# Kernel optimization log

Hardware: AMD Instinct MI355X
Metric: run time of the kernel (lower is better)

## Reference

```python
import jax, jax.numpy as jnp
import numpy as np

B, N, D = 1, 768, 768
H, HD = 16, 48
ZD = 128
EPS = 1e-5


def layer_norm(x, w, b):
    mu = jnp.mean(x, axis=-1, keepdims=True)
    var = jnp.mean(jnp.square(x - mu), axis=-1, keepdims=True)
    return (x - mu) * jax.lax.rsqrt(var + EPS) * w + b


def setup_inputs() -> dict:
    key = jax.random.key(0)
    ks = jax.random.split(key, 16)
    sc = 0.02
    return {
        "s": jax.random.normal(ks[0], (B, N, D), jnp.float32),
        "z": jax.random.normal(ks[1], (B, N, N, ZD), jnp.float32),
        "norm_s_w": jnp.ones((D,), jnp.float32),
        "norm_s_b": jnp.zeros((D,), jnp.float32),
        "q_w": jax.random.normal(ks[2], (D, D), jnp.float32) * sc,
        "q_b": jax.random.normal(ks[3], (D,), jnp.float32) * sc,
        "k_w": jax.random.normal(ks[4], (D, D), jnp.float32) * sc,
        "v_w": jax.random.normal(ks[5], (D, D), jnp.float32) * sc,
        "g_w": jax.random.normal(ks[6], (D, D), jnp.float32) * sc,
        "z_norm_w": jnp.ones((ZD,), jnp.float32),
        "z_norm_b": jnp.zeros((ZD,), jnp.float32),
        "z_w": jax.random.normal(ks[7], (ZD, H), jnp.float32) * sc,
        "o_w": jax.random.normal(ks[8], (D, D), jnp.float32) * sc,
    }


def reference(s, z, norm_s_w, norm_s_b, q_w, q_b, k_w, v_w, g_w,
              z_norm_w, z_norm_b, z_w, o_w):
    # diffusion=False: pre layer-norm on s
    sn = layer_norm(s, norm_s_w, norm_s_b)                 # [B,N,D]
    q = (sn @ q_w + q_b).reshape(B, N, H, HD)              # split D -> (H, HD)
    k = (sn @ k_w).reshape(B, N, H, HD)
    v = (sn @ v_w).reshape(B, N, H, HD)
    scale = HD ** -0.5
    # scores: [H,B,Q,K]
    a = jnp.einsum('bqhd,bkhd->hbqk', q, k) * scale
    # pair bias from z: LayerNorm + Linear(ZD->H), permute to [H,B,N,N]
    zb = layer_norm(z, z_norm_w, z_norm_b) @ z_w           # [B,N,N,H]
    a = a + jnp.transpose(zb, (3, 0, 1, 2))
    a = jax.nn.softmax(a, axis=-1)
    o = jnp.einsum('hbqk,bkhd->bqhd', a, v).reshape(B, N, D)
    g = jax.nn.sigmoid(sn @ g_w)                           # gate
    return (o * g) @ o_w
```

## Files before the change

### kernel.cpp

```cpp
#include <hip/hip_runtime.h>
#include <math.h>

constexpr int NT = 768;
constexpr int DT = 768;
constexpr int HT = 16;
constexpr int HDT = 48;
constexpr int ZDT = 128;
constexpr int NN = NT * NT;
constexpr float LN_EPS = 1e-5f;
constexpr float SCALE = 0.14433756729740643f;
constexpr int KP = 72;

typedef __attribute__((ext_vector_type(8))) short bfrag;
typedef __attribute__((ext_vector_type(4))) float ffrag;

#define MFMA16(a, b, c) __builtin_amdgcn_mfma_f32_16x16x32_bf16(a, b, c, 0, 0, 0)

__device__ __forceinline__ short f2b(float f) {
  unsigned u = __builtin_bit_cast(unsigned, f);
  u += 0x7fffu + ((u >> 16) & 1u);
  return (short)(u >> 16);
}
__device__ __forceinline__ float b2f(short s) {
  return __builtin_bit_cast(float, (unsigned)(unsigned short)s << 16);
}

__global__ __launch_bounds__(256) void ln_s_kernel(
    const float* __restrict__ s, const float* __restrict__ w,
    const float* __restrict__ b, short* __restrict__ snb) {
  const int row = blockIdx.x;
  const int t = threadIdx.x;
  const float* x = s + row * DT;
  float v0 = x[t], v1 = x[t + 256], v2 = x[t + 512];
  float sum = v0 + v1 + v2;
  float sq = v0 * v0 + v1 * v1 + v2 * v2;
#pragma unroll
  for (int off = 32; off; off >>= 1) {
    sum += __shfl_xor(sum, off);
    sq += __shfl_xor(sq, off);
  }
  __shared__ float ls[4], lq[4], stats[2];
  const int wid = t >> 6;
  if ((t & 63) == 0) { ls[wid] = sum; lq[wid] = sq; }
  __syncthreads();
  if (t == 0) {
    float S = ls[0] + ls[1] + ls[2] + ls[3];
    float Q = lq[0] + lq[1] + lq[2] + lq[3];
    float mu = S * (1.f / DT);
    float var = Q * (1.f / DT) - mu * mu;
    stats[0] = mu;
    stats[1] = rsqrtf(var + LN_EPS);
  }
  __syncthreads();
  const float mu = stats[0], rs = stats[1];
  short* y = snb + row * DT;
  y[t] = f2b((v0 - mu) * rs * w[t] + b[t]);
  y[t + 256] = f2b((v1 - mu) * rs * w[t + 256] + b[t + 256]);
  y[t + 512] = f2b((v2 - mu) * rs * w[t + 512] + b[t + 512]);
}

__global__ __launch_bounds__(256) void prep_kernel(
    const float* __restrict__ qw, const float* __restrict__ kw,
    const float* __restrict__ vw, const float* __restrict__ gw,
    const float* __restrict__ ow, short* __restrict__ wt) {
  __shared__ float Ts[64][65];
  const int t = threadIdx.x;
  const int which = blockIdx.z;
  const float* src = which == 0 ? qw : which == 1 ? kw : which == 2 ? vw
                     : which == 3 ? gw : ow;
  short* dst = wt + (size_t)which * NN;
  const int k0 = blockIdx.y * 64;
  const int n0 = blockIdx.x * 64;
  const int r = t >> 4, c = (t & 15) * 4;
#pragma unroll
  for (int i = 0; i < 4; i++) {
    int rr = r + i * 16;
    float4 v = *(const float4*)&src[(size_t)(k0 + rr) * DT + n0 + c];
    Ts[rr][c + 0] = v.x; Ts[rr][c + 1] = v.y;
    Ts[rr][c + 2] = v.z; Ts[rr][c + 3] = v.w;
  }
  __syncthreads();
#pragma unroll
  for (int i = 0; i < 2; i++) {
    int cid = t + i * 256;
    int nr = cid >> 3, kc = cid & 7;
    union { uint4 u; short s2[8]; } pk;
#pragma unroll
    for (int j = 0; j < 8; j++) pk.s2[j] = f2b(Ts[kc * 8 + j][nr]);
    *(uint4*)&dst[(size_t)(n0 + nr) * DT + k0 + kc * 8] = pk.u;
  }
}

__global__ __launch_bounds__(256) void zsetup_kernel(
    const float* __restrict__ znw, const float* __restrict__ znb,
    const float* __restrict__ zw, float* __restrict__ w1,
    float* __restrict__ bh) {
  const int t = threadIdx.x;
#pragma unroll
  for (int i = 0; i < 8; i++) {
    int idx = t * 8 + i;
    int c = idx >> 4;
    w1[idx] = znw[c] * zw[idx];
  }
  if (t < HT) {
    float s = 0.f;
    for (int c = 0; c < ZDT; c++) s += znb[c] * zw[c * HT + t];
    bh[t] = s;
  }
}

__global__ __launch_bounds__(256) void zbias_kernel(
    const float* __restrict__ z, const float* __restrict__ w1,
    const float* __restrict__ bh, short* __restrict__ biasb) {
  const int t = threadIdx.x;
  const int slot = t >> 5;
  const int hq = (t >> 3) & 3;
  const int cg = t & 7;
  const int c0 = cg * 16;
  const int h0 = hq * 4;
  float4 Wr[16];
#pragma unroll
  for (int j = 0; j < 16; j++)
    Wr[j] = *(const float4*)&w1[(c0 + j) * HT + h0];
  const float4 B4 = *(const float4*)&bh[h0];
  const int row0 = blockIdx.x * 256;
  for (int it = 0; it < 32; it++) {
    const int rid = row0 + it * 8 + slot;
    const float* zp = &z[(size_t)rid * ZDT + c0];
    float x[16];
    *(float4*)&x[0] = *(const float4*)&zp[0];
    *(float4*)&x[4] = *(const float4*)&zp[4];
    *(float4*)&x[8] = *(const float4*)&zp[8];
    *(float4*)&x[12] = *(const float4*)&zp[12];
    float sum = 0.f, sq = 0.f;
#pragma unroll
    for (int j = 0; j < 16; j++) { sum += x[j]; sq += x[j] * x[j]; }
#pragma unroll
    for (int m = 1; m <= 4; m <<= 1) {
      sum += __shfl_xor(sum, m);
      sq += __shfl_xor(sq, m);
    }
    const float mu = sum * (1.f / 128.f);
    const float rs = rsqrtf(sq * (1.f / 128.f) - mu * mu + LN_EPS);
    float ax = 0.f, ay = 0.f, az = 0.f, aw = 0.f;
#pragma unroll
    for (int j = 0; j < 16; j++) {
      float xc = x[j] - mu;
      ax += xc * Wr[j].x; ay += xc * Wr[j].y;
      az += xc * Wr[j].z; aw += xc * Wr[j].w;
    }
#pragma unroll
    for (int m = 1; m <= 4; m <<= 1) {
      ax += __shfl_xor(ax, m); ay += __shfl_xor(ay, m);
      az += __shfl_xor(az, m); aw += __shfl_xor(aw, m);
    }
    if (cg == 0) {
      biasb[(size_t)(h0 + 0) * NN + rid] = f2b(ax * rs + B4.x);
      biasb[(size_t)(h0 + 1) * NN + rid] = f2b(ay * rs + B4.y);
      biasb[(size_t)(h0 + 2) * NN + rid] = f2b(az * rs + B4.z);
      biasb[(size_t)(h0 + 3) * NN + rid] = f2b(aw * rs + B4.w);
    }
  }
}

__global__ __launch_bounds__(256) void proj_kernel(
    const short* __restrict__ snb, const short* __restrict__ wt,
    const float* __restrict__ qbias, short* __restrict__ qb,
    short* __restrict__ kb, short* __restrict__ vT, short* __restrict__ gb) {
  __shared__ short As[128 * KP];
  __shared__ short Bs[128 * KP];
  const int t = threadIdx.x;
  const int which = blockIdx.z;
  const short* W = wt + (size_t)which * NN;
  const int N0 = blockIdx.x * 128;
  const int M0 = blockIdx.y * 128;
  const int w = t >> 6, l = t & 63;
  const int wm = (w >> 1) * 64, wn = (w & 1) * 64;
  const int lane16 = l & 15, quad = l >> 4;
  ffrag acc[4][4] = {};
  const int srow = t >> 3, skc = t & 7;
  for (int k0 = 0; k0 < DT; k0 += 64) {
    uint4 av[4], bv[4];
#pragma unroll
    for (int i = 0; i < 4; i++) {
      int row = srow + i * 32;
      av[i] = *(const uint4*)&snb[(size_t)(M0 + row) * DT + k0 + skc * 8];
      bv[i] = *(const uint4*)&W[(size_t)(N0 + row) * DT + k0 + skc * 8];
    }
    __syncthreads();
#pragma unroll
    for (int i = 0; i < 4; i++) {
      int row = srow + i * 32;
      *(uint4*)&As[row * KP + skc * 8] = av[i];
      *(uint4*)&Bs[row * KP + skc * 8] = bv[i];
    }
    __syncthreads();
#pragma unroll
    for (int ks = 0; ks < 2; ks++) {
      bfrag a[4], b[4];
#pragma unroll
      for (int i = 0; i < 4; i++)
        a[i] = *(const bfrag*)&As[(wm + i * 16 + lane16) * KP + ks * 32 + quad * 8];
#pragma unroll
      for (int j = 0; j < 4; j++)
        b[j] = *(const bfrag*)&Bs[(wn + j * 16 + lane16) * KP + ks * 32 + quad * 8];
#pragma unroll
      for (int i = 0; i < 4; i++)
#pragma unroll
        for (int j = 0; j < 4; j++) acc[i][j] = MFMA16(a[i], b[j], acc[i][j]);
    }
    __syncthreads();
  }
#pragma unroll
  for (int i = 0; i < 4; i++) {
#pragma unroll
    for (int j = 0; j < 4; j++) {
      int n = N0 + wn + j * 16 + lane16;
#pragma unroll
      for (int r = 0; r < 4; r++) {
        int m = M0 + wm + i * 16 + quad * 4 + r;
        float v = acc[i][j][r];
        if (which == 0) {
          qb[(size_t)m * DT + n] = f2b(v + qbias[n]);
        } else if (which == 1) {
          kb[(size_t)m * DT + n] = f2b(v);
        } else if (which == 2) {
          vT[(size_t)n * NT + m] = f2b(v);
        } else {
          gb[(size_t)m * DT + n] = f2b(1.f / (1.f + __expf(-v)));
        }
      }
    }
  }
}

__global__ __launch_bounds__(256) void attn_kernel(
    const short* __restrict__ qb, const short* __restrict__ kb,
    const short* __restrict__ vT, const short* __restrict__ biasb,
    float* __restrict__ oX) {
  __shared__ short Ks[128 * 48];
  __shared__ short Vs[48 * 136];
  __shared__ short Ps[4][16 * 136];
  const int t = threadIdx.x;
  const int h = blockIdx.y;
  const int q0 = blockIdx.x * 64;
  const int w = t >> 6, l = t & 63;
  const int lane16 = l & 15, quad = l >> 4;
  const int qrow = q0 + w * 16 + lane16;
  bfrag a_q0 = *(const bfrag*)&qb[(size_t)qrow * DT + h * HDT + quad * 8];
  bfrag a_q1 = {0, 0, 0, 0, 0, 0, 0, 0};
  if (quad < 2)
    a_q1 = *(const bfrag*)&qb[(size_t)qrow * DT + h * HDT + 32 + quad * 8];
  const int koff1 = (quad < 2) ? (32 + quad * 8) : 0;
  ffrag acc_o[3] = {};
  float m_run[4] = {-1e30f, -1e30f, -1e30f, -1e30f};
  float l_run[4] = {};
  const size_t bias_base =
      (size_t)h * NN + (size_t)(q0 + w * 16 + quad * 4) * NT + lane16;
  for (int kt = 0; kt < 6; kt++) {
    const int k0 = kt * 128;
    uint4 kv[3], vv[3];
#pragma unroll
    for (int i = 0; i < 3; i++) {
      int cid = t + i * 256;
      int kr = cid / 6, kc = cid % 6;
      kv[i] = *(const uint4*)&kb[(size_t)(k0 + kr) * DT + h * HDT + kc * 8];
      int vr = cid >> 4, vc = cid & 15;
      vv[i] = *(const uint4*)&vT[((size_t)h * HDT + vr) * NT + k0 + vc * 8];
    }
    short bias_s[8][4];
#pragma unroll
    for (int j = 0; j < 8; j++)
#pragma unroll
      for (int r = 0; r < 4; r++)
        bias_s[j][r] = biasb[bias_base + (size_t)r * NT + k0 + j * 16];
    __syncthreads();
#pragma unroll
    for (int i = 0; i < 3; i++) {
      int cid = t + i * 256;
      int kr = cid / 6, kc = cid % 6;
      *(uint4*)&Ks[kr * 48 + kc * 8] = kv[i];
      int vr = cid >> 4, vc = cid & 15;
      *(uint4*)&Vs[vr * 136 + vc * 8] = vv[i];
    }
    __syncthreads();
    ffrag sc[8];
#pragma unroll
    for (int j = 0; j < 8; j++) {
      ffrag zf = {0.f, 0.f, 0.f, 0.f};
      bfrag b0 = *(const bfrag*)&Ks[(j * 16 + lane16) * 48 + quad * 8];
      bfrag b1 = *(const bfrag*)&Ks[(j * 16 + lane16) * 48 + koff1];
      zf = MFMA16(a_q0, b0, zf);
      sc[j] = MFMA16(a_q1, b1, zf);
    }
    float li[8][4];
#pragma unroll
    for (int j = 0; j < 8; j++)
#pragma unroll
      for (int r = 0; r < 4; r++)
        li[j][r] = sc[j][r] * SCALE + b2f(bias_s[j][r]);
    float alpha[4];
#pragma unroll
    for (int r = 0; r < 4; r++) {
      float m = li[0][r];
#pragma unroll
      for (int j = 1; j < 8; j++) m = fmaxf(m, li[j][r]);
#pragma unroll
      for (int k = 1; k <= 8; k <<= 1) m = fmaxf(m, __shfl_xor(m, k));
      float mn = fmaxf(m_run[r], m);
      alpha[r] = __expf(m_run[r] - mn);
      m_run[r] = mn;
    }
#pragma unroll
    for (int j = 0; j < 8; j++)
#pragma unroll
      for (int r = 0; r < 4; r++) li[j][r] = __expf(li[j][r] - m_run[r]);
#pragma unroll
    for (int r = 0; r < 4; r++) {
      float ssum = li[0][r];
#pragma unroll
      for (int j = 1; j < 8; j++) ssum += li[j][r];
#pragma unroll
      for (int k = 1; k <= 8; k <<= 1) ssum += __shfl_xor(ssum, k);
      l_run[r] = l_run[r] * alpha[r] + ssum;
    }
#pragma unroll
    for (int dt = 0; dt < 3; dt++)
#pragma unroll
      for (int r = 0; r < 4; r++) acc_o[dt][r] *= alpha[r];
#pragma unroll
    for (int j = 0; j < 8; j++)
#pragma unroll
      for (int r = 0; r < 4; r++)
        Ps[w][(quad * 4 + r) * 136 + j * 16 + lane16] = f2b(li[j][r]);
#pragma unroll
    for (int ks = 0; ks < 4; ks++) {
      bfrag ap = *(const bfrag*)&Ps[w][lane16 * 136 + ks * 32 + quad * 8];
#pragma unroll
      for (int dt = 0; dt < 3; dt++) {
        bfrag bv = *(const bfrag*)&Vs[(dt * 16 + lane16) * 136 + ks * 32 + quad * 8];
        acc_o[dt] = MFMA16(ap, bv, acc_o[dt]);
      }
    }
  }
  float inv[4];
#pragma unroll
  for (int r = 0; r < 4; r++) inv[r] = 1.f / l_run[r];
#pragma unroll
  for (int dt = 0; dt < 3; dt++)
#pragma unroll
    for (int r = 0; r < 4; r++)
      oX[(size_t)(q0 + w * 16 + quad * 4 + r) * DT + h * HDT + dt * 16 + lane16] =
          acc_o[dt][r] * inv[r];
}

__global__ __launch_bounds__(256) void outproj_kernel(
    const float* __restrict__ oX, const short* __restrict__ gb,
    const short* __restrict__ owt, float* __restrict__ out) {
  __shared__ short As[128 * KP];
  __shared__ short Bs[128 * KP];
  const int t = threadIdx.x;
  const int N0 = blockIdx.x * 128;
  const int M0 = blockIdx.y * 128;
  const int w = t >> 6, l = t & 63;
  const int wm = (w >> 1) * 64, wn = (w & 1) * 64;
  const int lane16 = l & 15, quad = l >> 4;
  ffrag acc[4][4] = {};
  const int srow = t >> 3, skc = t & 7;
  for (int k0 = 0; k0 < DT; k0 += 64) {
    uint4 apk[4], bvv[4];
#pragma unroll
    for (int i = 0; i < 4; i++) {
      int row = srow + i * 32;
      float4 o0 = *(const float4*)&oX[(size_t)(M0 + row) * DT + k0 + skc * 8];
      float4 o1 = *(const float4*)&oX[(size_t)(M0 + row) * DT + k0 + skc * 8 + 4];
      union { uint4 u; short s2[8]; } gv;
      gv.u = *(const uint4*)&gb[(size_t)(M0 + row) * DT + k0 + skc * 8];
      union { uint4 u; short s2[8]; } pk;
      float go[8] = {o0.x, o0.y, o0.z, o0.w, o1.x, o1.y, o1.z, o1.w};
#pragma unroll
      for (int jj = 0; jj < 8; jj++) pk.s2[jj] = f2b(go[jj] * b2f(gv.s2[jj]));
      apk[i] = pk.u;
      bvv[i] = *(const uint4*)&owt[(size_t)(N0 + row) * DT + k0 + skc * 8];
    }
    __syncthreads();
#pragma unroll
    for (int i = 0; i < 4; i++) {
      int row = srow + i * 32;
      *(uint4*)&As[row * KP + skc * 8] = apk[i];
      *(uint4*)&Bs[row * KP + skc * 8] = bvv[i];
    }
    __syncthreads();
#pragma unroll
    for (int ks = 0; ks < 2; ks++) {
      bfrag a[4], b[4];
#pragma unroll
      for (int i = 0; i < 4; i++)
        a[i] = *(const bfrag*)&As[(wm + i * 16 + lane16) * KP + ks * 32 + quad * 8];
#pragma unroll
      for (int j = 0; j < 4; j++)
        b[j] = *(const bfrag*)&Bs[(wn + j * 16 + lane16) * KP + ks * 32 + quad * 8];
#pragma unroll
      for (int i = 0; i < 4; i++)
#pragma unroll
        for (int j = 0; j < 4; j++) acc[i][j] = MFMA16(a[i], b[j], acc[i][j]);
    }
    __syncthreads();
  }
#pragma unroll
  for (int i = 0; i < 4; i++)
#pragma unroll
    for (int j = 0; j < 4; j++) {
      int n = N0 + wn + j * 16 + lane16;
#pragma unroll
      for (int r = 0; r < 4; r++) {
        int m = M0 + wm + i * 16 + quad * 4 + r;
        out[(size_t)m * DT + n] = acc[i][j][r];
      }
    }
}

extern "C" void kernel_launch(void* const* d_in, const int* in_sizes, int n_in,
                              void* d_out, int out_size, void* d_ws,
                              size_t ws_size, hipStream_t stream) {
  const float* s = (const float*)d_in[0];
  const float* z = (const float*)d_in[1];
  const float* nsw = (const float*)d_in[2];
  const float* nsb = (const float*)d_in[3];
  const float* qw = (const float*)d_in[4];
  const float* qbias = (const float*)d_in[5];
  const float* kw = (const float*)d_in[6];
  const float* vw = (const float*)d_in[7];
  const float* gw = (const float*)d_in[8];
  const float* znw = (const float*)d_in[9];
  const float* znb = (const float*)d_in[10];
  const float* zww = (const float*)d_in[11];
  const float* ow = (const float*)d_in[12];
  float* out = (float*)d_out;
  char* W = (char*)d_ws;

  short* biasb = (short*)W;
  short* snb = (short*)(W + 18874368);
  short* qb = (short*)(W + 20054016);
  short* kb = (short*)(W + 21233664);
  short* gb = (short*)(W + 22413312);
  short* vT = (short*)(W + 23592960);
  short* wt = (short*)(W + 24772608);
  float* oX = (float*)(W + 30670848);
  float* w1 = (float*)(W + 33030144);
  float* bh = (float*)(W + 33038336);

  ln_s_kernel<<<NT, 256, 0, stream>>>(s, nsw, nsb, snb);
  zsetup_kernel<<<1, 256, 0, stream>>>(znw, znb, zww, w1, bh);
  prep_kernel<<<dim3(12, 12, 5), 256, 0, stream>>>(qw, kw, vw, gw, ow, wt);
  zbias_kernel<<<2304, 256, 0, stream>>>(z, w1, bh, biasb);
  proj_kernel<<<dim3(6, 6, 4), 256, 0, stream>>>(snb, wt, qbias, qb, kb, vT, gb);
  attn_kernel<<<dim3(12, 16), 256, 0, stream>>>(qb, kb, vT, biasb, oX);
  outproj_kernel<<<dim3(6, 6), 256, 0, stream>>>(oX, gb, wt + 4 * (size_t)NN,
                                                 out);
}
```

Baseline: 599.9 us.

## Merge setup launches, co-schedule projection GEMM with z-bias, and retile out-projection

Three setup kernels (weight transpose, LayerNorm of s, z-weight folding) become one block-indexed launch. The projection GEMM and the z-bias kernel become a second launch, so the GEMM tiles run alongside the bandwidth-bound z streaming. The output projection moves from 128x128 to 64x64 tiles, giving 144 blocks instead of 36 to fill more CUs, and drops the redundant trailing barrier. The cost is larger combined kernels with branch-dependent register and LDS footprints, which may lower occupancy for the light paths.

```diff
diff --git a/kernel.cpp b/kernel.cpp
--- a/kernel.cpp
+++ b/kernel.cpp
@@ -25,210 +25,209 @@
   return __builtin_bit_cast(float, (unsigned)(unsigned short)s << 16);
 }
 
-__global__ __launch_bounds__(256) void ln_s_kernel(
-    const float* __restrict__ s, const float* __restrict__ w,
-    const float* __restrict__ b, short* __restrict__ snb) {
-  const int row = blockIdx.x;
-  const int t = threadIdx.x;
-  const float* x = s + row * DT;
-  float v0 = x[t], v1 = x[t + 256], v2 = x[t + 512];
-  float sum = v0 + v1 + v2;
-  float sq = v0 * v0 + v1 * v1 + v2 * v2;
-#pragma unroll
-  for (int off = 32; off; off >>= 1) {
-    sum += __shfl_xor(sum, off);
-    sq += __shfl_xor(sq, off);
-  }
-  __shared__ float ls[4], lq[4], stats[2];
-  const int wid = t >> 6;
-  if ((t & 63) == 0) { ls[wid] = sum; lq[wid] = sq; }
-  __syncthreads();
-  if (t == 0) {
-    float S = ls[0] + ls[1] + ls[2] + ls[3];
-    float Q = lq[0] + lq[1] + lq[2] + lq[3];
-    float mu = S * (1.f / DT);
-    float var = Q * (1.f / DT) - mu * mu;
-    stats[0] = mu;
-    stats[1] = rsqrtf(var + LN_EPS);
-  }
-  __syncthreads();
-  const float mu = stats[0], rs = stats[1];
-  short* y = snb + row * DT;
-  y[t] = f2b((v0 - mu) * rs * w[t] + b[t]);
-  y[t + 256] = f2b((v1 - mu) * rs * w[t + 256] + b[t + 256]);
-  y[t + 512] = f2b((v2 - mu) * rs * w[t + 512] + b[t + 512]);
-}
-
-__global__ __launch_bounds__(256) void prep_kernel(
+__global__ __launch_bounds__(256) void setup_kernel(
+    const float* __restrict__ s, const float* __restrict__ nsw,
+    const float* __restrict__ nsb, short* __restrict__ snb,
     const float* __restrict__ qw, const float* __restrict__ kw,
     const float* __restrict__ vw, const float* __restrict__ gw,
-    const float* __restrict__ ow, short* __restrict__ wt) {
-  __shared__ float Ts[64][65];
-  const int t = threadIdx.x;
-  const int which = blockIdx.z;
-  const float* src = which == 0 ? qw : which == 1 ? kw : which == 2 ? vw
-                     : which == 3 ? gw : ow;
-  short* dst = wt + (size_t)which * NN;
-  const int k0 = blockIdx.y * 64;
-  const int n0 = blockIdx.x * 64;
-  const int r = t >> 4, c = (t & 15) * 4;
-#pragma unroll
-  for (int i = 0; i < 4; i++) {
-    int rr = r + i * 16;
-    float4 v = *(const float4*)&src[(size_t)(k0 + rr) * DT + n0 + c];
-    Ts[rr][c + 0] = v.x; Ts[rr][c + 1] = v.y;
-    Ts[rr][c + 2] = v.z; Ts[rr][c + 3] = v.w;
-  }
-  __syncthreads();
-#pragma unroll
-  for (int i = 0; i < 2; i++) {
-    int cid = t + i * 256;
-    int nr = cid >> 3, kc = cid & 7;
-    union { uint4 u; short s2[8]; } pk;
-#pragma unroll
-    for (int j = 0; j < 8; j++) pk.s2[j] = f2b(Ts[kc * 8 + j][nr]);
-    *(uint4*)&dst[(size_t)(n0 + nr) * DT + k0 + kc * 8] = pk.u;
-  }
-}
-
-__global__ __launch_bounds__(256) void zsetup_kernel(
+    const float* __restrict__ ow, short* __restrict__ wt,
     const float* __restrict__ znw, const float* __restrict__ znb,
     const float* __restrict__ zw, float* __restrict__ w1,
     float* __restrict__ bh) {
+  const int bid = blockIdx.x;
   const int t = threadIdx.x;
-#pragma unroll
-  for (int i = 0; i < 8; i++) {
-    int idx = t * 8 + i;
-    int c = idx >> 4;
-    w1[idx] = znw[c] * zw[idx];
+  if (bid < 720) {
+    __shared__ float Ts[64][65];
+    const int which = bid / 144;
+    const int rem = bid % 144;
+    const int k0 = (rem / 12) * 64;
+    const int n0 = (rem % 12) * 64;
+    const float* src = which == 0 ? qw : which == 1 ? kw : which == 2 ? vw
+                       : which == 3 ? gw : ow;
+    short* dst = wt + (size_t)which * NN;
+    const int r = t >> 4, c = (t & 15) * 4;
+#pragma unroll
+    for (int i = 0; i < 4; i++) {
+      int rr = r + i * 16;
+      float4 v = *(const float4*)&src[(size_t)(k0 + rr) * DT + n0 + c];
+      Ts[rr][c + 0] = v.x; Ts[rr][c + 1] = v.y;
+      Ts[rr][c + 2] = v.z; Ts[rr][c + 3] = v.w;
+    }
+    __syncthreads();
+#pragma unroll
+    for (int i = 0; i < 2; i++) {
+      int cid = t + i * 256;
+      int nr = cid >> 3, kc = cid & 7;
+      union { uint4 u; short s2[8]; } pk;
+#pragma unroll
+      for (int j = 0; j < 8; j++) pk.s2[j] = f2b(Ts[kc * 8 + j][nr]);
+      *(uint4*)&dst[(size_t)(n0 + nr) * DT + k0 + kc * 8] = pk.u;
+    }
+  } else if (bid < 1488) {
+    const int row = bid - 720;
+    const float* x = s + row * DT;
+    float v0 = x[t], v1 = x[t + 256], v2 = x[t + 512];
+    float sum = v0 + v1 + v2;
+    float sq = v0 * v0 + v1 * v1 + v2 * v2;
+#pragma unroll
+    for (int off = 32; off; off >>= 1) {
+      sum += __shfl_xor(sum, off);
+      sq += __shfl_xor(sq, off);
+    }
+    __shared__ float ls[4], lq[4], stats[2];
+    const int wid = t >> 6;
+    if ((t & 63) == 0) { ls[wid] = sum; lq[wid] = sq; }
+    __syncthreads();
+    if (t == 0) {
+      float S = ls[0] + ls[1] + ls[2] + ls[3];
+      float Q = lq[0] + lq[1] + lq[2] + lq[3];
+      float mu = S * (1.f / DT);
+      float var = Q * (1.f / DT) - mu * mu;
+      stats[0] = mu;
+      stats[1] = rsqrtf(var + LN_EPS);
+    }
+    __syncthreads();
+    const float mu = stats[0], rs = stats[1];
+    short* y = snb + row * DT;
+    y[t] = f2b((v0 - mu) * rs * nsw[t] + nsb[t]);
+    y[t + 256] = f2b((v1 - mu) * rs * nsw[t + 256] + nsb[t + 256]);
+    y[t + 512] = f2b((v2 - mu) * rs * nsw[t + 512] + nsb[t + 512]);
+  } else {
+#pragma unroll
+    for (int i = 0; i < 8; i++) {
+      int idx = t * 8 + i;
+      int c = idx >> 4;
+      w1[idx] = znw[c] * zw[idx];
+    }
+    if (t < HT) {
+      float sv = 0.f;
+      for (int c = 0; c < ZDT; c++) sv += znb[c] * zw[c * HT + t];
+      bh[t] = sv;
+    }
   }
-  if (t < HT) {
-    float s = 0.f;
-    for (int c = 0; c < ZDT; c++) s += znb[c] * zw[c * HT + t];
-    bh[t] = s;
-  }
-}
-
-__global__ __launch_bounds__(256) void zbias_kernel(
+}
+
+__global__ __launch_bounds__(256) void zbias_proj_kernel(
+    const short* __restrict__ snb, const short* __restrict__ wt,
+    const float* __restrict__ qbias, short* __restrict__ qb,
+    short* __restrict__ kb, short* __restrict__ vT, short* __restrict__ gb,
     const float* __restrict__ z, const float* __restrict__ w1,
     const float* __restrict__ bh, short* __restrict__ biasb) {
+  const int bid = blockIdx.x;
   const int t = threadIdx.x;
-  const int slot = t >> 5;
-  const int hq = (t >> 3) & 3;
-  const int cg = t & 7;
-  const int c0 = cg * 16;
-  const int h0 = hq * 4;
-  float4 Wr[16];
-#pragma unroll
-  for (int j = 0; j < 16; j++)
-    Wr[j] = *(const float4*)&w1[(c0 + j) * HT + h0];
-  const float4 B4 = *(const float4*)&bh[h0];
-  const int row0 = blockIdx.x * 256;
-  for (int it = 0; it < 32; it++) {
-    const int rid = row0 + it * 8 + slot;
-    const float* zp = &z[(size_t)rid * ZDT + c0];
-    float x[16];
-    *(float4*)&x[0] = *(const float4*)&zp[0];
-    *(float4*)&x[4] = *(const float4*)&zp[4];
-    *(float4*)&x[8] = *(const float4*)&zp[8];
-    *(float4*)&x[12] = *(const float4*)&zp[12];
-    float sum = 0.f, sq = 0.f;
-#pragma unroll
-    for (int j = 0; j < 16; j++) { sum += x[j]; sq += x[j] * x[j]; }
-#pragma unroll
-    for (int m = 1; m <= 4; m <<= 1) {
-      sum += __shfl_xor(sum, m);
-      sq += __shfl_xor(sq, m);
-    }
-    const float mu = sum * (1.f / 128.f);
-    const float rs = rsqrtf(sq * (1.f / 128.f) - mu * mu + LN_EPS);
-    float ax = 0.f, ay = 0.f, az = 0.f, aw = 0.f;
-#pragma unroll
-    for (int j = 0; j < 16; j++) {
-      float xc = x[j] - mu;
-      ax += xc * Wr[j].x; ay += xc * Wr[j].y;
-      az += xc * Wr[j].z; aw += xc * Wr[j].w;
-    }
-#pragma unroll
-    for (int m = 1; m <= 4; m <<= 1) {
-      ax += __shfl_xor(ax, m); ay += __shfl_xor(ay, m);
-      az += __shfl_xor(az, m); aw += __shfl_xor(aw, m);
-    }
-    if (cg == 0) {
-      biasb[(size_t)(h0 + 0) * NN + rid] = f2b(ax * rs + B4.x);
-      biasb[(size_t)(h0 + 1) * NN + rid] = f2b(ay * rs + B4.y);
-      biasb[(size_t)(h0 + 2) * NN + rid] = f2b(az * rs + B4.z);
-      biasb[(size_t)(h0 + 3) * NN + rid] = f2b(aw * rs + B4.w);
-    }
-  }
-}
-
-__global__ __launch_bounds__(256) void proj_kernel(
-    const short* __restrict__ snb, const short* __restrict__ wt,
-    const float* __restrict__ qbias, short* __restrict__ qb,
-    short* __restrict__ kb, short* __restrict__ vT, short* __restrict__ gb) {
-  __shared__ short As[128 * KP];
-  __shared__ short Bs[128 * KP];
-  const int t = threadIdx.x;
-  const int which = blockIdx.z;
-  const short* W = wt + (size_t)which * NN;
-  const int N0 = blockIdx.x * 128;
-  const int M0 = blockIdx.y * 128;
-  const int w = t >> 6, l = t & 63;
-  const int wm = (w >> 1) * 64, wn = (w & 1) * 64;
-  const int lane16 = l & 15, quad = l >> 4;
-  ffrag acc[4][4] = {};
-  const int srow = t >> 3, skc = t & 7;
-  for (int k0 = 0; k0 < DT; k0 += 64) {
-    uint4 av[4], bv[4];
+  if (bid < 144) {
+    __shared__ short As[128 * KP];
+    __shared__ short Bs[128 * KP];
+    const int which = bid / 36;
+    const int rem = bid % 36;
+    const int N0 = (rem % 6) * 128;
+    const int M0 = (rem / 6) * 128;
+    const short* W = wt + (size_t)which * NN;
+    const int w = t >> 6, l = t & 63;
+    const int wm = (w >> 1) * 64, wn = (w & 1) * 64;
+    const int lane16 = l & 15, quad = l >> 4;
+    ffrag acc[4][4] = {};
+    const int srow = t >> 3, skc = t & 7;
+    for (int k0 = 0; k0 < DT; k0 += 64) {
+      uint4 av[4], bv[4];
+#pragma unroll
+      for (int i = 0; i < 4; i++) {
+        int row = srow + i * 32;
+        av[i] = *(const uint4*)&snb[(size_t)(M0 + row) * DT + k0 + skc * 8];
+        bv[i] = *(const uint4*)&W[(size_t)(N0 + row) * DT + k0 + skc * 8];
+      }
+      __syncthreads();
+#pragma unroll
+      for (int i = 0; i < 4; i++) {
+        int row = srow + i * 32;
+        *(uint4*)&As[row * KP + skc * 8] = av[i];
+        *(uint4*)&Bs[row * KP + skc * 8] = bv[i];
+      }
+      __syncthreads();
+#pragma unroll
+      for (int ks = 0; ks < 2; ks++) {
+        bfrag a[4], b[4];
+#pragma unroll
+        for (int i = 0; i < 4; i++)
+          a[i] = *(const bfrag*)&As[(wm + i * 16 + lane16) * KP + ks * 32 + quad * 8];
+#pragma unroll
+        for (int j = 0; j < 4; j++)
+          b[j] = *(const bfrag*)&Bs[(wn + j * 16 + lane16) * KP + ks * 32 + quad * 8];
+#pragma unroll
+        for (int i = 0; i < 4; i++)
+#pragma unroll
+          for (int j = 0; j < 4; j++) acc[i][j] = MFMA16(a[i], b[j], acc[i][j]);
+      }
+      __syncthreads();
+    }
 #pragma unroll
     for (int i = 0; i < 4; i++) {
-      int row = srow + i * 32;
-      av[i] = *(const uint4*)&snb[(size_t)(M0 + row) * DT + k0 + skc * 8];
-      bv[i] = *(const uint4*)&W[(size_t)(N0 + row) * DT + k0 + skc * 8];
-    }
-    __syncthreads();
-#pragma unroll
-    for (int i = 0; i < 4; i++) {
-      int row = srow + i * 32;
-      *(uint4*)&As[row * KP + skc * 8] = av[i];
-      *(uint4*)&Bs[row * KP + skc * 8] = bv[i];
-    }
-    __syncthreads();
-#pragma unroll
-    for (int ks = 0; ks < 2; ks++) {
-      bfrag a[4], b[4];
-#pragma unroll
-      for (int i = 0; i < 4; i++)
-        a[i] = *(const bfrag*)&As[(wm + i * 16 + lane16) * KP + ks * 32 + quad * 8];
-#pragma unroll
-      for (int j = 0; j < 4; j++)
-        b[j] = *(const bfrag*)&Bs[(wn + j * 16 + lane16) * KP + ks * 32 + quad * 8];
-#pragma unroll
-      for (int i = 0; i < 4; i++)
-#pragma unroll
-        for (int j = 0; j < 4; j++) acc[i][j] = MFMA16(a[i], b[j], acc[i][j]);
-    }
-    __syncthreads();
-  }
-#pragma unroll
-  for (int i = 0; i < 4; i++) {
-#pragma unroll
-    for (int j = 0; j < 4; j++) {
-      int n = N0 + wn + j * 16 + lane16;
-#pragma unroll
-      for (int r = 0; r < 4; r++) {
-        int m = M0 + wm + i * 16 + quad * 4 + r;
-        float v = acc[i][j][r];
-        if (which == 0) {
-          qb[(size_t)m * DT + n] = f2b(v + qbias[n]);
-        } else if (which == 1) {
-          kb[(size_t)m * DT + n] = f2b(v);
-        } else if (which == 2) {
-          vT[(size_t)n * NT + m] = f2b(v);
-        } else {
-          gb[(size_t)m * DT + n] = f2b(1.f / (1.f + __expf(-v)));
+#pragma unroll
+      for (int j = 0; j < 4; j++) {
+        int n = N0 + wn + j * 16 + lane16;
+#pragma unroll
+        for (int r = 0; r < 4; r++) {
+          int m = M0 + wm + i * 16 + quad * 4 + r;
+          float v = acc[i][j][r];
+          if (which == 0) {
+            qb[(size_t)m * DT + n] = f2b(v + qbias[n]);
+          } else if (which == 1) {
+            kb[(size_t)m * DT + n] = f2b(v);
+          } else if (which == 2) {
+            vT[(size_t)n * NT + m] = f2b(v);
+          } else {
+            gb[(size_t)m * DT + n] = f2b(1.f / (1.f + __expf(-v)));
+          }
         }
+      }
+    }
+  } else {
+    const int slot = t >> 5;
+    const int hq = (t >> 3) & 3;
+    const int cg = t & 7;
+    const int c0 = cg * 16;
+    const int h0 = hq * 4;
+    float4 Wr[16];
+#pragma unroll
+    for (int j = 0; j < 16; j++)
+      Wr[j] = *(const float4*)&w1[(c0 + j) * HT + h0];
+    const float4 B4 = *(const float4*)&bh[h0];
+    const int row0 = (bid - 144) * 256;
+    for (int it = 0; it < 32; it++) {
+      const int rid = row0 + it * 8 + slot;
+      const float* zp = &z[(size_t)rid * ZDT + c0];
+      float x[16];
+      *(float4*)&x[0] = *(const float4*)&zp[0];
+      *(float4*)&x[4] = *(const float4*)&zp[4];
+      *(float4*)&x[8] = *(const float4*)&zp[8];
+      *(float4*)&x[12] = *(const float4*)&zp[12];
+      float sum = 0.f, sq = 0.f;
+#pragma unroll
+      for (int j = 0; j < 16; j++) { sum += x[j]; sq += x[j] * x[j]; }
+#pragma unroll
+      for (int m = 1; m <= 4; m <<= 1) {
+        sum += __shfl_xor(sum, m);
+        sq += __shfl_xor(sq, m);
+      }
+      const float mu = sum * (1.f / 128.f);
+      const float rs = rsqrtf(sq * (1.f / 128.f) - mu * mu + LN_EPS);
+      float ax = 0.f, ay = 0.f, az = 0.f, aw = 0.f;
+#pragma unroll
+      for (int j = 0; j < 16; j++) {
+        float xc = x[j] - mu;
+        ax += xc * Wr[j].x; ay += xc * Wr[j].y;
+        az += xc * Wr[j].z; aw += xc * Wr[j].w;
+      }
+#pragma unroll
+      for (int m = 1; m <= 4; m <<= 1) {
+        ax += __shfl_xor(ax, m); ay += __shfl_xor(ay, m);
+        az += __shfl_xor(az, m); aw += __shfl_xor(aw, m);
+      }
+      if (cg == 0) {
+        biasb[(size_t)(h0 + 0) * NN + rid] = f2b(ax * rs + B4.x);
+        biasb[(size_t)(h0 + 1) * NN + rid] = f2b(ay * rs + B4.y);
+        biasb[(size_t)(h0 + 2) * NN + rid] = f2b(az * rs + B4.z);
+        biasb[(size_t)(h0 + 3) * NN + rid] = f2b(aw * rs + B4.w);
       }
     }
   }
@@ -357,60 +356,60 @@
 __global__ __launch_bounds__(256) void outproj_kernel(
     const float* __restrict__ oX, const short* __restrict__ gb,
     const short* __restrict__ owt, float* __restrict__ out) {
-  __shared__ short As[128 * KP];
-  __shared__ short Bs[128 * KP];
+  __shared__ short As[64 * KP];
+  __shared__ short Bs[64 * KP];
   const int t = threadIdx.x;
-  const int N0 = blockIdx.x * 128;
-  const int M0 = blockIdx.y * 128;
+  const int N0 = blockIdx.x * 64;
+  const int M0 = blockIdx.y * 64;
   const int w = t >> 6, l = t & 63;
-  const int wm = (w >> 1) * 64, wn = (w & 1) * 64;
+  const int wm = (w >> 1) * 32, wn = (w & 1) * 32;
   const int lane16 = l & 15, quad = l >> 4;
-  ffrag acc[4][4] = {};
-  const int srow = t >> 3, skc = t & 7;
+  ffrag acc[2][2] = {};
+  const int srow = t >> 2;
+  const int sc = (t & 3) * 16;
   for (int k0 = 0; k0 < DT; k0 += 64) {
-    uint4 apk[4], bvv[4];
-#pragma unroll
-    for (int i = 0; i < 4; i++) {
-      int row = srow + i * 32;
-      float4 o0 = *(const float4*)&oX[(size_t)(M0 + row) * DT + k0 + skc * 8];
-      float4 o1 = *(const float4*)&oX[(size_t)(M0 + row) * DT + k0 + skc * 8 + 4];
+    uint4 apk[2], bvv[2];
+    const float* op = &oX[(size_t)(M0 + srow) * DT + k0 + sc];
+    const short* gp = &gb[(size_t)(M0 + srow) * DT + k0 + sc];
+    const short* bp = &owt[(size_t)(N0 + srow) * DT + k0 + sc];
+#pragma unroll
+    for (int i = 0; i < 2; i++) {
+      float4 o0 = *(const float4*)&op[i * 8 + 0];
+      float4 o1 = *(const float4*)&op[i * 8 + 4];
       union { uint4 u; short s2[8]; } gv;
-      gv.u = *(const uint4*)&gb[(size_t)(M0 + row) * DT + k0 + skc * 8];
+      gv.u = *(const uint4*)&gp[i * 8];
       union { uint4 u; short s2[8]; } pk;
       float go[8] = {o0.x, o0.y, o0.z, o0.w, o1.x, o1.y, o1.z, o1.w};
 #pragma unroll
       for (int jj = 0; jj < 8; jj++) pk.s2[jj] = f2b(go[jj] * b2f(gv.s2[jj]));
       apk[i] = pk.u;
-      bvv[i] = *(const uint4*)&owt[(size_t)(N0 + row) * DT + k0 + skc * 8];
-    }
-    __syncthreads();
-#pragma unroll
-    for (int i = 0; i < 4; i++) {
-      int row = srow + i * 32;
-      *(uint4*)&As[row * KP + skc * 8] = apk[i];
-      *(uint4*)&Bs[row * KP + skc * 8] = bvv[i];
-    }
+      bvv[i] = *(const uint4*)&bp[i * 8];
+    }
+    __syncthreads();
+    *(uint4*)&As[srow * KP + sc] = apk[0];
+    *(uint4*)&As[srow * KP + sc + 8] = apk[1];
+    *(uint4*)&Bs[srow * KP + sc] = bvv[0];
+    *(uint4*)&Bs[srow * KP + sc + 8] = bvv[1];
     __syncthreads();
 #pragma unroll
     for (int ks = 0; ks < 2; ks++) {
-      bfrag a[4], b[4];
-#pragma unroll
-      for (int i = 0; i < 4; i++)
+      bfrag a[2], b[2];
+#pragma unroll
+      for (int i = 0; i < 2; i++)
         a[i] = *(const bfrag*)&As[(wm + i * 16 + lane16) * KP + ks * 32 + quad * 8];
 #pragma unroll
-      for (int j = 0; j < 4; j++)
+      for (int j = 0; j < 2; j++)
         b[j] = *(const bfrag*)&Bs[(wn + j * 16 + lane16) * KP + ks * 32 + quad * 8];
 #pragma unroll
-      for (int i = 0; i < 4; i++)
-#pragma unroll
-        for (int j = 0; j < 4; j++) acc[i][j] = MFMA16(a[i], b[j], acc[i][j]);
-    }
-    __syncthreads();
+      for (int i = 0; i < 2; i++)
+#pragma unroll
+        for (int j = 0; j < 2; j++) acc[i][j] = MFMA16(a[i], b[j], acc[i][j]);
+    }
   }
 #pragma unroll
-  for (int i = 0; i < 4; i++)
-#pragma unroll
-    for (int j = 0; j < 4; j++) {
+  for (int i = 0; i < 2; i++)
+#pragma unroll
+    for (int j = 0; j < 2; j++) {
       int n = N0 + wn + j * 16 + lane16;
 #pragma unroll
       for (int r = 0; r < 4; r++) {
@@ -450,12 +449,11 @@
   float* w1 = (float*)(W + 33030144);
   float* bh = (float*)(W + 33038336);
 
-  ln_s_kernel<<<NT, 256, 0, stream>>>(s, nsw, nsb, snb);
-  zsetup_kernel<<<1, 256, 0, stream>>>(znw, znb, zww, w1, bh);
-  prep_kernel<<<dim3(12, 12, 5), 256, 0, stream>>>(qw, kw, vw, gw, ow, wt);
-  zbias_kernel<<<2304, 256, 0, stream>>>(z, w1, bh, biasb);
-  proj_kernel<<<dim3(6, 6, 4), 256, 0, stream>>>(snb, wt, qbias, qb, kb, vT, gb);
+  setup_kernel<<<1489, 256, 0, stream>>>(s, nsw, nsb, snb, qw, kw, vw, gw, ow,
+                                         wt, znw, znb, zww, w1, bh);
+  zbias_proj_kernel<<<2448, 256, 0, stream>>>(snb, wt, qbias, qb, kb, vT, gb,
+                                              z, w1, bh, biasb);
   attn_kernel<<<dim3(12, 16), 256, 0, stream>>>(qb, kb, vT, biasb, oX);
-  outproj_kernel<<<dim3(6, 6), 256, 0, stream>>>(oX, gb, wt + 4 * (size_t)NN,
-                                                 out);
-}
+  outproj_kernel<<<dim3(12, 12), 256, 0, stream>>>(oX, gb, wt + 4 * (size_t)NN,
+                                                   out);
+}
```

After: 622.9 us. +3.8%, slower.
